# Performance work log

Measured on AMD Instinct MI355X. Metric: run time of the kernel, lower is better.

## Reference

```python
import jax, jax.numpy as jnp
import numpy as np

B, T, D, H, HS = 4, 2048, 512, 8, 64

def setup_inputs() -> dict:
    key = jax.random.key(0)
    ks = jax.random.split(key, 5)
    scale = 1.0 / np.sqrt(D)
    return {
        "x": jax.random.normal(ks[0], (B, T, D), dtype=jnp.float32),
        "Wq": jax.random.normal(ks[1], (H, D, HS), dtype=jnp.float32) * scale,
        "Wk": jax.random.normal(ks[2], (H, D, HS), dtype=jnp.float32) * scale,
        "Wv": jax.random.normal(ks[3], (H, D, HS), dtype=jnp.float32) * scale,
        "Wo": jax.random.normal(ks[4], (D, D), dtype=jnp.float32) * scale,
        "bo": jnp.zeros((D,), dtype=jnp.float32),
    }

def reference(x, Wq, Wk, Wv, Wo, bo):
    # Per-head projections (stacked heads) -> [B,H,T,HS]
    q = jnp.einsum('btd,hde->bhte', x, Wq)
    k = jnp.einsum('btd,hde->bhte', x, Wk)
    v = jnp.einsum('btd,hde->bhte', x, Wv)
    # Full TxT attention scores, scaled by head_size**-0.5
    scores = jnp.einsum('bhte,bhse->bhts', q, k) * (HS ** -0.5)
    att = jax.nn.softmax(scores, axis=-1)
    out = jnp.einsum('bhts,bhse->bhte', att, v)
    # Concat heads: [B,H,T,HS] -> [B,T,H*HS] == [B,T,D]
    out = jnp.transpose(out, (0, 2, 1, 3)).reshape(out.shape[0], out.shape[2], -1)
    # Output projection (nn.Linear with bias)
    return out @ Wo + bo
```

## Files before the change

kernel.cpp:

```cpp
#include <hip/hip_runtime.h>
#include <stdint.h>

#define B_   4
#define T_   2048
#define D_   512
#define H_   8
#define HS_  64

typedef __attribute__((ext_vector_type(8))) short bf16x8;
typedef __attribute__((ext_vector_type(4))) float f32x4;

__device__ __forceinline__ unsigned short f2bf(float f) {
  union { float f; unsigned u; } v; v.f = f;
  unsigned r = v.u + 0x7fffu + ((v.u >> 16) & 1u);
  return (unsigned short)(r >> 16);
}

__device__ __forceinline__ void gload_lds16(const void* g, void* l) {
  __builtin_amdgcn_global_load_lds(
      (const __attribute__((address_space(1))) void*)g,
      (__attribute__((address_space(3))) void*)l,
      16, 0, 0);
}

__global__ __launch_bounds__(256) void k_prep(
    const float* __restrict__ x,
    const float* __restrict__ Wq, const float* __restrict__ Wk,
    const float* __restrict__ Wv, const float* __restrict__ Wo,
    unsigned short* __restrict__ xb, unsigned short* __restrict__ Wtq,
    unsigned short* __restrict__ Wto)
{
  const int bid = blockIdx.x, tid = threadIdx.x;
  if (bid < 4096) {
    const int i = bid * 256 + tid;
    float4 v = ((const float4*)x)[i];
    ushort4 o;
    o.x = f2bf(v.x); o.y = f2bf(v.y); o.z = f2bf(v.z); o.w = f2bf(v.w);
    ((ushort4*)xb)[i] = o;
  } else if (bid < 7168) {
    const int idx = (bid - 4096) * 256 + tid;
    const int n = idx >> 9, d = idx & 511;
    const int proj = n >> 9, c = n & 511, h = c >> 6, e = c & 63;
    const float* W = (proj == 0) ? Wq : ((proj == 1) ? Wk : Wv);
    Wtq[idx] = f2bf(W[((h << 9) + d) * 64 + e]);
  } else {
    const int idx = (bid - 7168) * 256 + tid;
    const int n = idx >> 9, d = idx & 511;
    Wto[idx] = f2bf(Wo[(d << 9) + n]);
  }
}

template<int MODE>
__global__ __launch_bounds__(256) void k_gemm(
    const unsigned short* __restrict__ A, const unsigned short* __restrict__ Bt,
    unsigned short* __restrict__ Qb, unsigned short* __restrict__ Kb,
    unsigned short* __restrict__ Vp,
    const float* __restrict__ bo, float* __restrict__ Cout)
{
  const int m0 = blockIdx.y * 128, n0 = blockIdx.x * 128;
  __shared__ unsigned short At[128 * 32];
  __shared__ unsigned short Bs[128 * 32];
  const int tid = threadIdx.x, lane = tid & 63, wid = tid >> 6;
  const int wm = wid >> 1, wn = wid & 1;
  const int r16 = lane & 15, g = lane >> 4;

  f32x4 acc[4][4];
  const f32x4 fz = {0.f, 0.f, 0.f, 0.f};
#pragma unroll
  for (int i = 0; i < 4; ++i)
#pragma unroll
    for (int j = 0; j < 4; ++j) acc[i][j] = fz;

  for (int k0 = 0; k0 < 512; k0 += 32) {
#pragma unroll
    for (int j = 0; j < 2; ++j) {
      const int idx = j * 256 + tid;
      const int rr = idx >> 2, cc = (idx & 3) << 3;
      gload_lds16(A + (size_t)(m0 + rr) * 512 + k0 + cc, &At[(j * 256 + wid * 64) * 8]);
      gload_lds16(Bt + (size_t)(n0 + rr) * 512 + k0 + cc, &Bs[(j * 256 + wid * 64) * 8]);
    }
    __syncthreads();
    bf16x8 am[4], bn[4];
#pragma unroll
    for (int mi = 0; mi < 4; ++mi)
      am[mi] = *(const bf16x8*)&At[(wm * 64 + mi * 16 + r16) * 32 + g * 8];
#pragma unroll
    for (int ni = 0; ni < 4; ++ni)
      bn[ni] = *(const bf16x8*)&Bs[(wn * 64 + ni * 16 + r16) * 32 + g * 8];
#pragma unroll
    for (int mi = 0; mi < 4; ++mi)
#pragma unroll
      for (int ni = 0; ni < 4; ++ni)
        acc[mi][ni] = __builtin_amdgcn_mfma_f32_16x16x32_bf16(am[mi], bn[ni], acc[mi][ni], 0, 0, 0);
    __syncthreads();
  }

  const float QSC = 0.18033688f;
#pragma unroll
  for (int mi = 0; mi < 4; ++mi) {
#pragma unroll
    for (int ni = 0; ni < 4; ++ni) {
#pragma unroll
      for (int r = 0; r < 4; ++r) {
        const int m = m0 + wm * 64 + mi * 16 + g * 4 + r;
        const int n = n0 + wn * 64 + ni * 16 + r16;
        const float val = acc[mi][ni][r];
        if (MODE == 0) {
          const int proj = n >> 9, c = n & 511, h = c >> 6, e = c & 63;
          const int b = m >> 11, t = m & 2047;
          if (proj == 0) {
            Qb[(((size_t)(b * 8 + h) * 2048 + t) << 6) + e] = f2bf(val * QSC);
          } else if (proj == 1) {
            Kb[(((size_t)(b * 8 + h) * 2048 + t) << 6) + e] = f2bf(val);
          } else {
            const int kk = t & 31, tblk = t >> 5;
            const int j = (((kk >> 2) & 3) << 3) + ((kk >> 4) << 2) + (kk & 3);
            Vp[(((size_t)(b * 8 + h) << 6) + e) * 2048 + (tblk << 5) + j] = f2bf(val);
          }
        } else {
          Cout[(size_t)m * 512 + n] = val + bo[n];
        }
      }
    }
  }
}

#define WAITBAR4() do { \
    asm volatile("s_waitcnt vmcnt(4)" ::: "memory"); \
    __builtin_amdgcn_s_barrier(); \
    asm volatile("" ::: "memory"); } while (0)
#define WAITBAR0() do { \
    asm volatile("s_waitcnt vmcnt(0)" ::: "memory"); \
    __builtin_amdgcn_s_barrier(); \
    asm volatile("" ::: "memory"); } while (0)
#define ENDBAR() do { \
    asm volatile("" ::: "memory"); \
    __builtin_amdgcn_s_barrier(); \
    asm volatile("" ::: "memory"); } while (0)

__global__ __launch_bounds__(256, 4) void k_attn(
    const unsigned short* __restrict__ Qb, const unsigned short* __restrict__ Kb,
    const unsigned short* __restrict__ Vp, unsigned short* __restrict__ Ob)
{
  const int lin = blockIdx.x;
  const int xcd = lin & 7, slot = lin >> 3;
  const int bh = xcd * 4 + (slot & 3);
  const int qblk = slot >> 2;
  const int b = bh >> 3, h = bh & 7;

  const int tid = threadIdx.x, lane = tid & 63, wid = tid >> 6;
  const int q0 = qblk * 64 + wid * 16;
  const int r16 = lane & 15, g = lane >> 4;
  const int swz = r16 & 7;
  const unsigned short* Qh = Qb + (size_t)bh * T_ * 64;
  const unsigned short* Kh = Kb + (size_t)bh * T_ * 64;
  const unsigned short* Vh = Vp + (size_t)bh * 64 * T_;

  __shared__ unsigned short Ks[2][4096];
  __shared__ unsigned short Vs[2][4096];

  const bf16x8 qa0 = *(const bf16x8*)&Qh[(size_t)(q0 + r16) * 64 + g * 8];
  const bf16x8 qa1 = *(const bf16x8*)&Qh[(size_t)(q0 + r16) * 64 + 32 + g * 8];

  const f32x4 fz = {0.f, 0.f, 0.f, 0.f};
  f32x4 acc[4];
#pragma unroll
  for (int eb = 0; eb < 4; ++eb) acc[eb] = fz;
  f32x4 accL = fz;

  bf16x8 onesv;
#pragma unroll
  for (int i = 0; i < 8; ++i) onesv[i] = (short)0x3F80;

  const int sb = wid * 8 + (lane >> 3);
  const int ssc = (lane & 7) ^ (lane >> 3);
  const unsigned short* kg = Kh + (size_t)sb * 64 + ssc * 8;
  const unsigned short* vg = Vh + (size_t)sb * T_ + ssc * 8;

  auto stage = [&](const unsigned short* kgp, const unsigned short* vgp, int bf) {
    gload_lds16(kgp,                  &Ks[bf][wid * 512]);
    gload_lds16(kgp + 32 * 64,        &Ks[bf][2048 + wid * 512]);
    gload_lds16(vgp,                  &Vs[bf][wid * 512]);
    gload_lds16(vgp + (size_t)32 * T_, &Vs[bf][2048 + wid * 512]);
  };

  auto compute = [&](int bf) {
#pragma unroll
    for (int sub = 0; sub < 2; ++sub) {
      const int rb = (sub * 32 + r16) * 64;
      const int c0 = (g ^ swz) << 3;
      const bf16x8 kf00 = *(const bf16x8*)&Ks[bf][rb + c0];
      const bf16x8 kf01 = *(const bf16x8*)&Ks[bf][rb + (c0 ^ 32)];
      const bf16x8 kf10 = *(const bf16x8*)&Ks[bf][rb + 1024 + c0];
      const bf16x8 kf11 = *(const bf16x8*)&Ks[bf][rb + 1024 + (c0 ^ 32)];
      f32x4 s0 = __builtin_amdgcn_mfma_f32_16x16x32_bf16(kf00, qa0, fz, 0, 0, 0);
      s0 = __builtin_amdgcn_mfma_f32_16x16x32_bf16(kf01, qa1, s0, 0, 0, 0);
      f32x4 s1 = __builtin_amdgcn_mfma_f32_16x16x32_bf16(kf10, qa0, fz, 0, 0, 0);
      s1 = __builtin_amdgcn_mfma_f32_16x16x32_bf16(kf11, qa1, s1, 0, 0, 0);

      float p[8];
#pragma unroll
      for (int r = 0; r < 4; ++r) {
        p[r]     = exp2f(s0[r]);
        p[4 + r] = exp2f(s1[r]);
      }
      union { bf16x8 v; unsigned u[4]; } pu;
#pragma unroll
      for (int i = 0; i < 4; ++i)
        asm("v_cvt_pk_bf16_f32 %0, %1, %2" : "=v"(pu.u[i]) : "v"(p[2 * i]), "v"(p[2 * i + 1]));

#pragma unroll
      for (int eb = 0; eb < 4; ++eb) {
        const bf16x8 vf = *(const bf16x8*)&Vs[bf][(eb * 16 + r16) * 64 + (c0 ^ (sub << 5))];
        acc[eb] = __builtin_amdgcn_mfma_f32_16x16x32_bf16(vf, pu.v, acc[eb], 0, 0, 0);
      }
      accL = __builtin_amdgcn_mfma_f32_16x16x32_bf16(onesv, pu.v, accL, 0, 0, 0);
    }
  };

  stage(kg, vg, 0); kg += 4096; vg += 64;
#pragma unroll 1
  for (int t = 0; t < 30; t += 2) {
    stage(kg, vg, 1); kg += 4096; vg += 64;
    WAITBAR4();
    compute(0);
    ENDBAR();
    stage(kg, vg, 0); kg += 4096; vg += 64;
    WAITBAR4();
    compute(1);
    ENDBAR();
  }
  stage(kg, vg, 1);
  WAITBAR4();
  compute(0);
  ENDBAR();
  WAITBAR0();
  compute(1);

  const float invL = 1.0f / accL[0];
  unsigned short* Orow = Ob + ((size_t)(b * 2048 + q0 + r16) << 9) + h * 64 + g * 4;
#pragma unroll
  for (int eb = 0; eb < 4; ++eb) {
    uint2 ow;
    asm("v_cvt_pk_bf16_f32 %0, %1, %2" : "=v"(ow.x)
        : "v"(acc[eb][0] * invL), "v"(acc[eb][1] * invL));
    asm("v_cvt_pk_bf16_f32 %0, %1, %2" : "=v"(ow.y)
        : "v"(acc[eb][2] * invL), "v"(acc[eb][3] * invL));
    *(uint2*)(Orow + eb * 16) = ow;
  }
}

extern "C" void kernel_launch(void* const* d_in, const int* in_sizes, int n_in,
                              void* d_out, int out_size, void* d_ws, size_t ws_size,
                              hipStream_t stream) {
  const float* x  = (const float*)d_in[0];
  const float* Wq = (const float*)d_in[1];
  const float* Wk = (const float*)d_in[2];
  const float* Wv = (const float*)d_in[3];
  const float* Wo = (const float*)d_in[4];
  const float* bo = (const float*)d_in[5];
  float* out = (float*)d_out;
  char* ws = (char*)d_ws;

  unsigned short* xb  = (unsigned short*)(ws);
  unsigned short* Wtq = (unsigned short*)(ws + 8388608);
  unsigned short* Wto = (unsigned short*)(ws + 9961472);
  unsigned short* Qb  = (unsigned short*)(ws + 10485760);
  unsigned short* Kb  = (unsigned short*)(ws + 18874368);
  unsigned short* Vp  = (unsigned short*)(ws + 27262976);
  unsigned short* Ob  = (unsigned short*)(ws + 35651584);

  k_prep    <<<8192, 256, 0, stream>>>(x, Wq, Wk, Wv, Wo, xb, Wtq, Wto);
  k_gemm<0> <<<dim3(12, 64), 256, 0, stream>>>(xb, Wtq, Qb, Kb, Vp, nullptr, nullptr);
  k_attn    <<<1024, 256, 0, stream>>>(Qb, Kb, Vp, Ob);
  k_gemm<1> <<<dim3(4, 64), 256, 0, stream>>>(Ob, Wto, nullptr, nullptr, nullptr, bo, out);
}
```

Measured before the change: 110.2 us.

## Process 32 query rows per wave in attention to reuse K/V tiles

Each wave in the attention kernel now handles two 16-row query tiles, so every K and V fragment loaded from LDS feeds twice as many MFMAs. The grid halves to 512 blocks and launch bounds drop to 3 blocks per SM to leave room for the doubled accumulators. The double-buffer sync also changes from partial vmcnt waits plus separate end barriers to one full drain and barrier per stage, which may expose more load latency. Fewer blocks also means less parallelism across CUs.

```diff
diff --git a/kernel.cpp b/kernel.cpp
--- a/kernel.cpp
+++ b/kernel.cpp
@@ -125,20 +125,12 @@
   }
 }
 
-#define WAITBAR4() do { \
-    asm volatile("s_waitcnt vmcnt(4)" ::: "memory"); \
-    __builtin_amdgcn_s_barrier(); \
-    asm volatile("" ::: "memory"); } while (0)
-#define WAITBAR0() do { \
+#define DRAINBAR() do { \
     asm volatile("s_waitcnt vmcnt(0)" ::: "memory"); \
     __builtin_amdgcn_s_barrier(); \
     asm volatile("" ::: "memory"); } while (0)
-#define ENDBAR() do { \
-    asm volatile("" ::: "memory"); \
-    __builtin_amdgcn_s_barrier(); \
-    asm volatile("" ::: "memory"); } while (0)
-
-__global__ __launch_bounds__(256, 4) void k_attn(
+
+__global__ __launch_bounds__(256, 3) void k_attn(
     const unsigned short* __restrict__ Qb, const unsigned short* __restrict__ Kb,
     const unsigned short* __restrict__ Vp, unsigned short* __restrict__ Ob)
 {
@@ -149,7 +141,7 @@
   const int b = bh >> 3, h = bh & 7;
 
   const int tid = threadIdx.x, lane = tid & 63, wid = tid >> 6;
-  const int q0 = qblk * 64 + wid * 16;
+  const int q0 = qblk * 128 + wid * 32;
   const int r16 = lane & 15, g = lane >> 4;
   const int swz = r16 & 7;
   const unsigned short* Qh = Qb + (size_t)bh * T_ * 64;
@@ -159,14 +151,16 @@
   __shared__ unsigned short Ks[2][4096];
   __shared__ unsigned short Vs[2][4096];
 
-  const bf16x8 qa0 = *(const bf16x8*)&Qh[(size_t)(q0 + r16) * 64 + g * 8];
-  const bf16x8 qa1 = *(const bf16x8*)&Qh[(size_t)(q0 + r16) * 64 + 32 + g * 8];
+  const bf16x8 qa00 = *(const bf16x8*)&Qh[(size_t)(q0 + r16) * 64 + g * 8];
+  const bf16x8 qa01 = *(const bf16x8*)&Qh[(size_t)(q0 + r16) * 64 + 32 + g * 8];
+  const bf16x8 qa10 = *(const bf16x8*)&Qh[(size_t)(q0 + 16 + r16) * 64 + g * 8];
+  const bf16x8 qa11 = *(const bf16x8*)&Qh[(size_t)(q0 + 16 + r16) * 64 + 32 + g * 8];
 
   const f32x4 fz = {0.f, 0.f, 0.f, 0.f};
-  f32x4 acc[4];
-#pragma unroll
-  for (int eb = 0; eb < 4; ++eb) acc[eb] = fz;
-  f32x4 accL = fz;
+  f32x4 accA[4], accB[4];
+#pragma unroll
+  for (int eb = 0; eb < 4; ++eb) { accA[eb] = fz; accB[eb] = fz; }
+  f32x4 accLA = fz, accLB = fz;
 
   bf16x8 onesv;
 #pragma unroll
@@ -178,9 +172,9 @@
   const unsigned short* vg = Vh + (size_t)sb * T_ + ssc * 8;
 
   auto stage = [&](const unsigned short* kgp, const unsigned short* vgp, int bf) {
-    gload_lds16(kgp,                  &Ks[bf][wid * 512]);
-    gload_lds16(kgp + 32 * 64,        &Ks[bf][2048 + wid * 512]);
-    gload_lds16(vgp,                  &Vs[bf][wid * 512]);
+    gload_lds16(kgp,                   &Ks[bf][wid * 512]);
+    gload_lds16(kgp + 32 * 64,         &Ks[bf][2048 + wid * 512]);
+    gload_lds16(vgp,                   &Vs[bf][wid * 512]);
     gload_lds16(vgp + (size_t)32 * T_, &Vs[bf][2048 + wid * 512]);
   };
 
@@ -193,60 +187,71 @@
       const bf16x8 kf01 = *(const bf16x8*)&Ks[bf][rb + (c0 ^ 32)];
       const bf16x8 kf10 = *(const bf16x8*)&Ks[bf][rb + 1024 + c0];
       const bf16x8 kf11 = *(const bf16x8*)&Ks[bf][rb + 1024 + (c0 ^ 32)];
-      f32x4 s0 = __builtin_amdgcn_mfma_f32_16x16x32_bf16(kf00, qa0, fz, 0, 0, 0);
-      s0 = __builtin_amdgcn_mfma_f32_16x16x32_bf16(kf01, qa1, s0, 0, 0, 0);
-      f32x4 s1 = __builtin_amdgcn_mfma_f32_16x16x32_bf16(kf10, qa0, fz, 0, 0, 0);
-      s1 = __builtin_amdgcn_mfma_f32_16x16x32_bf16(kf11, qa1, s1, 0, 0, 0);
-
-      float p[8];
+      f32x4 s0a = __builtin_amdgcn_mfma_f32_16x16x32_bf16(kf00, qa00, fz, 0, 0, 0);
+      s0a = __builtin_amdgcn_mfma_f32_16x16x32_bf16(kf01, qa01, s0a, 0, 0, 0);
+      f32x4 s1a = __builtin_amdgcn_mfma_f32_16x16x32_bf16(kf10, qa00, fz, 0, 0, 0);
+      s1a = __builtin_amdgcn_mfma_f32_16x16x32_bf16(kf11, qa01, s1a, 0, 0, 0);
+      f32x4 s0b = __builtin_amdgcn_mfma_f32_16x16x32_bf16(kf00, qa10, fz, 0, 0, 0);
+      s0b = __builtin_amdgcn_mfma_f32_16x16x32_bf16(kf01, qa11, s0b, 0, 0, 0);
+      f32x4 s1b = __builtin_amdgcn_mfma_f32_16x16x32_bf16(kf10, qa10, fz, 0, 0, 0);
+      s1b = __builtin_amdgcn_mfma_f32_16x16x32_bf16(kf11, qa11, s1b, 0, 0, 0);
+
+      float pa[8], pb[8];
 #pragma unroll
       for (int r = 0; r < 4; ++r) {
-        p[r]     = exp2f(s0[r]);
-        p[4 + r] = exp2f(s1[r]);
-      }
-      union { bf16x8 v; unsigned u[4]; } pu;
-#pragma unroll
-      for (int i = 0; i < 4; ++i)
-        asm("v_cvt_pk_bf16_f32 %0, %1, %2" : "=v"(pu.u[i]) : "v"(p[2 * i]), "v"(p[2 * i + 1]));
+        pa[r]     = exp2f(s0a[r]);
+        pa[4 + r] = exp2f(s1a[r]);
+        pb[r]     = exp2f(s0b[r]);
+        pb[4 + r] = exp2f(s1b[r]);
+      }
+      union { bf16x8 v; unsigned u[4]; } puA, puB;
+#pragma unroll
+      for (int i = 0; i < 4; ++i) {
+        asm("v_cvt_pk_bf16_f32 %0, %1, %2" : "=v"(puA.u[i]) : "v"(pa[2 * i]), "v"(pa[2 * i + 1]));
+        asm("v_cvt_pk_bf16_f32 %0, %1, %2" : "=v"(puB.u[i]) : "v"(pb[2 * i]), "v"(pb[2 * i + 1]));
+      }
 
 #pragma unroll
       for (int eb = 0; eb < 4; ++eb) {
         const bf16x8 vf = *(const bf16x8*)&Vs[bf][(eb * 16 + r16) * 64 + (c0 ^ (sub << 5))];
-        acc[eb] = __builtin_amdgcn_mfma_f32_16x16x32_bf16(vf, pu.v, acc[eb], 0, 0, 0);
-      }
-      accL = __builtin_amdgcn_mfma_f32_16x16x32_bf16(onesv, pu.v, accL, 0, 0, 0);
+        accA[eb] = __builtin_amdgcn_mfma_f32_16x16x32_bf16(vf, puA.v, accA[eb], 0, 0, 0);
+        accB[eb] = __builtin_amdgcn_mfma_f32_16x16x32_bf16(vf, puB.v, accB[eb], 0, 0, 0);
+      }
+      accLA = __builtin_amdgcn_mfma_f32_16x16x32_bf16(onesv, puA.v, accLA, 0, 0, 0);
+      accLB = __builtin_amdgcn_mfma_f32_16x16x32_bf16(onesv, puB.v, accLB, 0, 0, 0);
     }
   };
 
   stage(kg, vg, 0); kg += 4096; vg += 64;
+  DRAINBAR();
+
 #pragma unroll 1
-  for (int t = 0; t < 30; t += 2) {
+  for (int t = 0; t < 32; t += 2) {
     stage(kg, vg, 1); kg += 4096; vg += 64;
-    WAITBAR4();
     compute(0);
-    ENDBAR();
-    stage(kg, vg, 0); kg += 4096; vg += 64;
-    WAITBAR4();
+    DRAINBAR();
+    if (t < 30) { stage(kg, vg, 0); kg += 4096; vg += 64; }
     compute(1);
-    ENDBAR();
-  }
-  stage(kg, vg, 1);
-  WAITBAR4();
-  compute(0);
-  ENDBAR();
-  WAITBAR0();
-  compute(1);
-
-  const float invL = 1.0f / accL[0];
-  unsigned short* Orow = Ob + ((size_t)(b * 2048 + q0 + r16) << 9) + h * 64 + g * 4;
+    DRAINBAR();
+  }
+
+  const float invLA = 1.0f / accLA[0];
+  const float invLB = 1.0f / accLB[0];
+  unsigned short* OrowA = Ob + ((size_t)(b * 2048 + q0 + r16) << 9) + h * 64 + g * 4;
+  unsigned short* OrowB = Ob + ((size_t)(b * 2048 + q0 + 16 + r16) << 9) + h * 64 + g * 4;
 #pragma unroll
   for (int eb = 0; eb < 4; ++eb) {
     uint2 ow;
     asm("v_cvt_pk_bf16_f32 %0, %1, %2" : "=v"(ow.x)
-        : "v"(acc[eb][0] * invL), "v"(acc[eb][1] * invL));
+        : "v"(accA[eb][0] * invLA), "v"(accA[eb][1] * invLA));
     asm("v_cvt_pk_bf16_f32 %0, %1, %2" : "=v"(ow.y)
-        : "v"(acc[eb][2] * invL), "v"(acc[eb][3] * invL));
-    *(uint2*)(Orow + eb * 16) = ow;
+        : "v"(accA[eb][2] * invLA), "v"(accA[eb][3] * invLA));
+    *(uint2*)(OrowA + eb * 16) = ow;
+    asm("v_cvt_pk_bf16_f32 %0, %1, %2" : "=v"(ow.x)
+        : "v"(accB[eb][0] * invLB), "v"(accB[eb][1] * invLB));
+    asm("v_cvt_pk_bf16_f32 %0, %1, %2" : "=v"(ow.y)
+        : "v"(accB[eb][2] * invLB), "v"(accB[eb][3] * invLB));
+    *(uint2*)(OrowB + eb * 16) = ow;
   }
 }
 
@@ -272,6 +277,6 @@
 
   k_prep    <<<8192, 256, 0, stream>>>(x, Wq, Wk, Wv, Wo, xb, Wtq, Wto);
   k_gemm<0> <<<dim3(12, 64), 256, 0, stream>>>(xb, Wtq, Qb, Kb, Vp, nullptr, nullptr);
-  k_attn    <<<1024, 256, 0, stream>>>(Qb, Kb, Vp, Ob);
+  k_attn    <<<512, 256, 0, stream>>>(Qb, Kb, Vp, Ob);
   k_gemm<1> <<<dim3(4, 64), 256, 0, stream>>>(Ob, Wto, nullptr, nullptr, nullptr, bo, out);
 }
```

After: 110.3 us. About the same (+0.1%).
